# Optimization experiments

Hardware: AMD Instinct MI355X
Metric: run time of the kernel (lower is better)

## Reference

```python
import jax, jax.numpy as jnp
import numpy as np

N = 256        # SSM state size
D_MODEL = 2048 # number of independent channels sharing the kernel
L_MAX = 4096   # sequence length


def setup_inputs() -> dict:
    key = jax.random.key(0)
    k1, k2, k3, k4 = jax.random.split(key, 4)
    s = float(np.sqrt(N))
    # Stable A: eigenvalues with negative real part so A^l stays bounded after
    # bilinear discretization with step = 1/L.
    A = 0.5 * jax.random.normal(k1, (N, N), jnp.float32) / s - jnp.eye(N, dtype=jnp.float32)
    B = jax.random.normal(k2, (N, 1), jnp.float32) / s   # lecun-scale
    C = jax.random.normal(k3, (1, N), jnp.float32) / s
    D = jnp.ones((1,), jnp.float32)
    y = jax.random.normal(k4, (D_MODEL, L_MAX), jnp.float32)
    return {"y": y, "A": A, "B": B, "C": C, "D": D}


def _build_kernel(A, B, C, L, step):
    # Bilinear (Tustin) discretization, as in discretize_SSM.
    I = jnp.eye(A.shape[0], dtype=A.dtype)
    BL = jnp.linalg.inv(I - (step / 2.0) * A)
    Abar = BL @ (I + (step / 2.0) * A)
    Bbar = (BL * step) @ B                      # (N, 1)
    # K[l] = C @ Abar^l @ Bbar, computed as L matvecs via scan
    # (same math as the matrix_power loop, without O(L*N^3) cost).
    def step_fn(x, _):
        return Abar @ x, (C @ x)[0]
    _, K = jax.lax.scan(step_fn, Bbar[:, 0], None, length=L)
    return K                                     # (L,)


def _causal_conv(y, K):
    # mode='full' convolution truncated to first L samples == causal conv.
    L = y.shape[-1]
    n = 2 * L
    Yf = jnp.fft.rfft(y, n=n, axis=-1)           # (d_model, n//2+1)
    Kf = jnp.fft.rfft(K, n=n)                    # (n//2+1,)
    return jnp.fft.irfft(Yf * Kf, n=n, axis=-1)[..., :L]


def reference(y, A, B, C, D):
    L = y.shape[-1]
    K = _build_kernel(A, B, C, L, step=1.0 / L)
    return _causal_conv(y, K) + D * y
```

## Files before the change

### kernel.cpp

```cpp
#include <hip/hip_runtime.h>

#define N_ 256
#define L_ 4096
#define DM_ 2048
#define STEPF (1.0f / 4096.0f)
#define NW 15
#define NV 6
#define RQN 4608

typedef short bf16x8 __attribute__((ext_vector_type(8)));
typedef float f32x4 __attribute__((ext_vector_type(4)));
typedef unsigned int uint32;

__device__ __forceinline__ uint32 bf16rne(float f) {
    uint32 u = __builtin_bit_cast(uint32, f);
    return (u + 0x7FFFu + ((u >> 16) & 1u)) >> 16;
}
__device__ __forceinline__ float rdlane(float v, int l) {
    return __builtin_bit_cast(float, __builtin_amdgcn_readlane(__builtin_bit_cast(int, v), l));
}
__device__ __forceinline__ float hif(float x) {
    return __builtin_bit_cast(float, __builtin_bit_cast(uint32, x) & 0xFFFF0000u);
}
#define PK2(LO, HI) __builtin_amdgcn_perm(__builtin_bit_cast(uint32, (HI)), \
                                          __builtin_bit_cast(uint32, (LO)), 0x07060302u)

__global__ __launch_bounds__(1024) void k_build(const float* __restrict__ Araw,
                                                const float* __restrict__ Bv,
                                                const float* __restrict__ Cv,
                                                uint2* __restrict__ Rqg) {
    __shared__ float sm[39168];
    float* kry = sm;
    float* red = sm + 3840;
    float* Wl  = sm + 5888;
    float* Vt  = sm + 22528;
    float* Kf  = sm;

    const int tid = threadIdx.x;
    const int j = tid & 255, seg = tid >> 8, lane = tid & 63;
    const int e = 64 * seg + lane;
    float a[64];

#define DOT64(S0, S1, VV) { \
    _Pragma("unroll") \
    for (int m = 0; m < 64; m += 2) { \
        S0 = fmaf(rdlane(VV, m), a[m], S0); \
        S1 = fmaf(rdlane(VV, m + 1), a[m + 1], S1); \
    } }

#pragma unroll
    for (int m = 0; m < 64; ++m) a[m] = Araw[(64 * seg + m) * 256 + j];
    if (tid < 256) kry[tid] = Cv[tid];
    __syncthreads();
    const float WSC = 4032.0f / 4096.0f;
    {
        float vv = kry[e];
        for (int n = 1; n < NW; ++n) {
            float s0 = 0.f, s1 = 0.f;
            DOT64(s0, s1, vv)
            float* rb = red + (n & 1) * 1024;
            rb[seg * 256 + j] = s0 + s1;
            __syncthreads();
            float sc = WSC / (float)n;
            vv = (rb[e] + rb[256 + e] + rb[512 + e] + rb[768 + e]) * sc;
            if (tid < 256)
                kry[n * 256 + tid] = (rb[tid] + rb[256 + tid] + rb[512 + tid] + rb[768 + tid]) * sc;
        }
    }
    __syncthreads();
    {
        float kj[NW];
#pragma unroll
        for (int n = 0; n < NW; ++n) kj[n] = kry[n * 256 + j];
#pragma unroll
        for (int u = 0; u < 16; ++u) {
            int q = seg + 4 * u;
            float c = (float)q * (1.0f / 63.0f);
            float h = kj[NW - 1];
#pragma unroll
            for (int n = NW - 2; n >= 0; --n) h = fmaf(c, h, kj[n]);
            Wl[q * 260 + j] = h;
        }
    }

    {
        const float4* Ar = (const float4*)(Araw + (size_t)j * 256 + 64 * seg);
#pragma unroll
        for (int m4 = 0; m4 < 16; ++m4) {
            float4 q4 = Ar[m4];
            a[4 * m4] = q4.x; a[4 * m4 + 1] = q4.y; a[4 * m4 + 2] = q4.z; a[4 * m4 + 3] = q4.w;
        }
    }
    const float ms = 0.5f * STEPF;
    const float bve = Bv[e];
    {
        float vv = bve;
        for (int it = 0; it < 3; ++it) {
            float s0 = 0.f, s1 = 0.f;
            DOT64(s0, s1, vv)
            float* rb = red + (it & 1) * 1024;
            rb[seg * 256 + j] = s0 + s1;
            __syncthreads();
            vv = fmaf(ms, rb[e] + rb[256 + e] + rb[512 + e] + rb[768 + e], bve);
            if (it == 2 && tid < 256) {
                float su = rb[tid] + rb[256 + tid] + rb[512 + tid] + rb[768 + tid];
                kry[tid] = STEPF * fmaf(ms, su, Bv[tid]);
            }
        }
    }
    __syncthreads();
    const float VSC = 63.0f / 4096.0f;
    {
        float vv = kry[e];
        for (int n = 1; n < NV; ++n) {
            float s0 = 0.f, s1 = 0.f;
            DOT64(s0, s1, vv)
            float* rb = red + (n & 1) * 1024;
            rb[seg * 256 + j] = s0 + s1;
            __syncthreads();
            float sc = VSC / (float)n;
            vv = (rb[e] + rb[256 + e] + rb[512 + e] + rb[768 + e]) * sc;
            if (tid < 256)
                kry[n * 256 + tid] = (rb[tid] + rb[256 + tid] + rb[512 + tid] + rb[768 + tid]) * sc;
        }
    }
    __syncthreads();
    {
        float kj[NV];
#pragma unroll
        for (int n = 0; n < NV; ++n) kj[n] = kry[n * 256 + j];
#pragma unroll
        for (int u = 0; u < 16; ++u) {
            int r = seg + 4 * u;
            float c = (float)r * (1.0f / 63.0f);
            float h = kj[NV - 1];
#pragma unroll
            for (int n = NV - 2; n >= 0; --n) h = fmaf(c, h, kj[n]);
            Vt[r * 260 + j] = h;
        }
    }
    __syncthreads();

    {
        const int wv = tid >> 6;
        const int qt = wv >> 2, rt = wv & 3;
        const int n16 = lane & 15, g4 = lane >> 4;
        const int q = 16 * qt + n16;
        const int r = 16 * rt + n16;
        f32x4 ac = (f32x4){0.f, 0.f, 0.f, 0.f};
        for (int s = 0; s < 8; ++s) {
            const int kk = 32 * s + 8 * g4;
            float4 w0 = *(const float4*)&Wl[q * 260 + kk];
            float4 w1 = *(const float4*)&Wl[q * 260 + kk + 4];
            float4 v0 = *(const float4*)&Vt[r * 260 + kk];
            float4 v1 = *(const float4*)&Vt[r * 260 + kk + 4];
            uint4 uh; uh.x = PK2(w0.x, w0.y); uh.y = PK2(w0.z, w0.w);
                      uh.z = PK2(w1.x, w1.y); uh.w = PK2(w1.z, w1.w);
            float l0 = w0.x - hif(w0.x), l1 = w0.y - hif(w0.y);
            float l2 = w0.z - hif(w0.z), l3 = w0.w - hif(w0.w);
            float l4 = w1.x - hif(w1.x), l5 = w1.y - hif(w1.y);
            float l6 = w1.z - hif(w1.z), l7 = w1.w - hif(w1.w);
            uint4 ul; ul.x = PK2(l0, l1); ul.y = PK2(l2, l3);
                      ul.z = PK2(l4, l5); ul.w = PK2(l6, l7);
            uint4 uv; uv.x = PK2(v0.x, v0.y); uv.y = PK2(v0.z, v0.w);
                      uv.z = PK2(v1.x, v1.y); uv.w = PK2(v1.z, v1.w);
            ac = __builtin_amdgcn_mfma_f32_16x16x32_bf16(__builtin_bit_cast(bf16x8, uh),
                                                         __builtin_bit_cast(bf16x8, uv), ac, 0, 0, 0);
            ac = __builtin_amdgcn_mfma_f32_16x16x32_bf16(__builtin_bit_cast(bf16x8, ul),
                                                         __builtin_bit_cast(bf16x8, uv), ac, 0, 0, 0);
        }
#pragma unroll
        for (int jj = 0; jj < 4; ++jj)
            Kf[(16 * qt + 4 * g4 + jj) * 64 + r] = ac[jj];
    }
    __syncthreads();

    for (int i = tid; i < RQN; i += 1024) {
        int aa = 4095 - i;
        uint32 e0 = (aa >= 0) ? bf16rne(Kf[aa]) : 0u;
        uint32 e1 = (aa >= 1) ? bf16rne(Kf[aa - 1]) : 0u;
        uint32 e2 = (aa >= 2) ? bf16rne(Kf[aa - 2]) : 0u;
        uint32 e3 = (aa >= 3) ? bf16rne(Kf[aa - 3]) : 0u;
        uint2 v; v.x = e0 | (e1 << 16); v.y = e2 | (e3 << 16);
        Rqg[i] = v;
    }
#undef DOT64
}

__global__ __launch_bounds__(256, 2) void k_conv(const uint2* __restrict__ Rqg,
                                                 const float* __restrict__ y,
                                                 const float* __restrict__ Dp,
                                                 float* __restrict__ out) {
    __shared__ uint2 Rq[RQN];
    __shared__ f32x4 mbuf[2][8][64];
    const int tid = threadIdx.x;
#pragma unroll
    for (int i = 0; i < RQN / 256; ++i) Rq[i * 256 + tid] = Rqg[i * 256 + tid];
    __syncthreads();

    const int w = tid >> 6, lane = tid & 63;
    const int n = lane & 15, g = lane >> 4;
    const int ds = w & 1, jh = w >> 1;
    const int by = (int)blockIdx.y;
    const int d0w = (int)blockIdx.x * 32 + ds * 16;
    const int d = d0w + n;
    const float4* __restrict__ yq = (const float4*)(y + (size_t)d * L_);
    const float D0 = Dp[0];

#define LOADF(SL, I0) { \
    uint2 u0 = Rq[(I0)]; uint2 u1 = Rq[(I0) + 4]; \
    uint4 uu; uu.x = u0.x; uu.y = u0.y; uu.z = u1.x; uu.w = u1.y; \
    fr[SL] = __builtin_bit_cast(bf16x8, uu); }
#define PACKAV(Q0, Q1) { \
    uint4 ua; ua.x = PK2((Q0).x, (Q0).y); ua.y = PK2((Q0).z, (Q0).w); \
    ua.z = PK2((Q1).x, (Q1).y); ua.w = PK2((Q1).z, (Q1).w); \
    av = __builtin_bit_cast(bf16x8, ua); }
#define MF(TI, SL) acc[TI] = __builtin_amdgcn_mfma_f32_16x16x32_bf16(av, fr[SL], acc[TI], 0, 0, 0);

#define STEPB(YI, S0,S1,S2,S3,S4,S5,S6,S7,S8,S9,S10,S11,S12,S13,S14,S15) { \
    PACKAV(q0a, q0b); \
    q0a = q1a; q0b = q1b; \
    MF(14, S14) MF(15, S15) \
    LOADF(S14, bcur + 32) LOADF(S15, bcur + 16) \
    q1a = yq[(YI)]; q1b = yq[(YI) + 1]; \
    yn += 8; bcur += 32; \
    MF(0,S0) MF(1,S1) MF(2,S2) MF(3,S3) MF(4,S4) MF(5,S5) MF(6,S6) MF(7,S7) \
    MF(8,S8) MF(9,S9) MF(10,S10) MF(11,S11) MF(12,S12) MF(13,S13) \
}

#define ROUND8(YIM) \
    STEPB(YIM, 0,1,2,3,4,5,6,7,8,9,10,11,12,13,14,15) \
    STEPB(YIM, 14,15,0,1,2,3,4,5,6,7,8,9,10,11,12,13) \
    STEPB(YIM, 12,13,14,15,0,1,2,3,4,5,6,7,8,9,10,11) \
    STEPB(YIM, 10,11,12,13,14,15,0,1,2,3,4,5,6,7,8,9) \
    STEPB(YIM, 8,9,10,11,12,13,14,15,0,1,2,3,4,5,6,7) \
    STEPB(YIM, 6,7,8,9,10,11,12,13,14,15,0,1,2,3,4,5) \
    STEPB(YIM, 4,5,6,7,8,9,10,11,12,13,14,15,0,1,2,3) \
    STEPB(YIM, 2,3,4,5,6,7,8,9,10,11,12,13,14,15,0,1)

#define ROUND4(YIM) \
    STEPB(YIM, 0,1,2,3,4,5,6,7,8,9,10,11,12,13,14,15) \
    STEPB(YIM, 14,15,0,1,2,3,4,5,6,7,8,9,10,11,12,13) \
    STEPB(YIM, 12,13,14,15,0,1,2,3,4,5,6,7,8,9,10,11) \
    STEPB(YIM, 10,11,12,13,14,15,0,1,2,3,4,5,6,7,8,9)

    for (int strip = 0; strip < 2; ++strip) {
        const int v = strip ? by : (15 - by);
        const int t0 = v << 8;
        const int Sh = 4 * (v + 1);
        const int s0 = jh * Sh;

        f32x4 acc[16];
#pragma unroll
        for (int i = 0; i < 16; ++i) acc[i] = (f32x4){0.f, 0.f, 0.f, 0.f};
        bf16x8 fr[16], av;
        float4 q0a, q0b, q1a, q1b;

        const int B0 = 4095 - t0 - n + 8 * g + 32 * s0;
#pragma unroll
        for (int ti = 0; ti < 16; ++ti) LOADF(ti, B0 - 16 * ti)
        q0a = yq[8 * s0 + 2 * g];     q0b = yq[8 * s0 + 2 * g + 1];
        q1a = yq[8 * s0 + 8 + 2 * g]; q1b = yq[8 * s0 + 8 + 2 * g + 1];
        int bcur = B0;
        int yn = 8 * s0 + 16 + 2 * g;

        const int n8 = Sh >> 3;
        for (int it = 0; it < n8 - 1; ++it) {
            ROUND8(yn)
        }
        if (n8 > 0) {
            ROUND8(yn < 1016 ? yn : 1016)
        }
        if (Sh & 4) {
            ROUND4(yn)
        }

#pragma unroll
        for (int rr = 0; rr < 2; ++rr) {
            if (jh == 1) {
#pragma unroll
                for (int i = 0; i < 8; ++i) mbuf[ds][i][lane] = acc[rr * 8 + i];
            }
            __syncthreads();
            if (jh == 0) {
#pragma unroll
                for (int i = 0; i < 8; ++i) {
                    f32x4 m = mbuf[ds][i][lane];
                    acc[rr * 8 + i][0] += m[0]; acc[rr * 8 + i][1] += m[1];
                    acc[rr * 8 + i][2] += m[2]; acc[rr * 8 + i][3] += m[3];
                }
            }
            __syncthreads();
        }
        if (jh == 0) {
#pragma unroll
            for (int ti = 0; ti < 16; ++ti) {
                int tcol = t0 + 16 * ti + n;
#pragma unroll
                for (int r = 0; r < 4; ++r) {
                    int dr = d0w + 4 * g + r;
                    size_t ix = (size_t)dr * L_ + tcol;
                    out[ix] = acc[ti][r] + D0 * y[ix];
                }
            }
        }
    }

#undef ROUND8
#undef ROUND4
#undef STEPB
#undef MF
#undef PACKAV
#undef LOADF
}


extern "C" void kernel_launch(void* const* d_in, const int* in_sizes, int n_in,
                              void* d_out, int out_size, void* d_ws, size_t ws_size,
                              hipStream_t stream) {
    const float* y  = (const float*)d_in[0];
    const float* A  = (const float*)d_in[1];
    const float* Bv = (const float*)d_in[2];
    const float* Cv = (const float*)d_in[3];
    const float* Dp = (const float*)d_in[4];
    float* out = (float*)d_out;
    uint2* Rqg = (uint2*)d_ws;

    k_build<<<dim3(1), dim3(1024), 0, stream>>>(A, Bv, Cv, Rqg);
    k_conv<<<dim3(64, 8), dim3(256), 0, stream>>>(Rqg, y, Dp, out);

    (void)in_sizes; (void)n_in; (void)out_size; (void)ws_size;
}
```

Measured before the change: 79.92 us.

## Halve time tile to 128, widen blocks to 64 channels with 8 waves

The conv kernel now uses 512-thread blocks covering 64 channels (4 channel groups × 2 K-halves) and 128-sample output time tiles instead of 256. The grid becomes 32×16 with 16 triangular strip pairs. Each wave holds 8 accumulators and 8 Toeplitz fragments instead of 16, which lowers register pressure and allows more occupancy, and the staged Rq table in LDS is shared by more waves. In exchange each y load feeds fewer MFMAs, so reuse per load drops and there are more loop iterations and reductions.

New measurement: 107.3 us. +34.2%, slower.

```diff
diff --git a/kernel.cpp b/kernel.cpp
--- a/kernel.cpp
+++ b/kernel.cpp
@@ -187,22 +187,22 @@
 #undef DOT64
 }
 
-__global__ __launch_bounds__(256, 2) void k_conv(const uint2* __restrict__ Rqg,
+__global__ __launch_bounds__(512, 4) void k_conv(const uint2* __restrict__ Rqg,
                                                  const float* __restrict__ y,
                                                  const float* __restrict__ Dp,
                                                  float* __restrict__ out) {
     __shared__ uint2 Rq[RQN];
-    __shared__ f32x4 mbuf[2][8][64];
+    __shared__ f32x4 mbuf[4][8][64];
     const int tid = threadIdx.x;
 #pragma unroll
-    for (int i = 0; i < RQN / 256; ++i) Rq[i * 256 + tid] = Rqg[i * 256 + tid];
+    for (int i = 0; i < RQN / 512; ++i) Rq[i * 512 + tid] = Rqg[i * 512 + tid];
     __syncthreads();
 
     const int w = tid >> 6, lane = tid & 63;
     const int n = lane & 15, g = lane >> 4;
-    const int ds = w & 1, jh = w >> 1;
+    const int ds = w & 3, jh = w >> 2;
     const int by = (int)blockIdx.y;
-    const int d0w = (int)blockIdx.x * 32 + ds * 16;
+    const int d0w = (int)blockIdx.x * 64 + ds * 16;
     const int d = d0w + n;
     const float4* __restrict__ yq = (const float4*)(y + (size_t)d * L_);
     const float D0 = Dp[0];
@@ -217,84 +217,78 @@
     av = __builtin_bit_cast(bf16x8, ua); }
 #define MF(TI, SL) acc[TI] = __builtin_amdgcn_mfma_f32_16x16x32_bf16(av, fr[SL], acc[TI], 0, 0, 0);
 
-#define STEPB(YI, S0,S1,S2,S3,S4,S5,S6,S7,S8,S9,S10,S11,S12,S13,S14,S15) { \
+#define STEPE(YI, S0,S1,S2,S3,S4,S5,S6,S7) { \
     PACKAV(q0a, q0b); \
-    q0a = q1a; q0b = q1b; \
-    MF(14, S14) MF(15, S15) \
-    LOADF(S14, bcur + 32) LOADF(S15, bcur + 16) \
+    MF(6, S6) MF(7, S7) \
+    LOADF(S6, bcur + 32) LOADF(S7, bcur + 16) \
+    q0a = yq[(YI)]; q0b = yq[(YI) + 1]; \
+    yn += 8; bcur += 32; \
+    MF(0,S0) MF(1,S1) MF(2,S2) MF(3,S3) MF(4,S4) MF(5,S5) \
+}
+#define STEPO(YI, S0,S1,S2,S3,S4,S5,S6,S7) { \
+    PACKAV(q1a, q1b); \
+    MF(6, S6) MF(7, S7) \
+    LOADF(S6, bcur + 32) LOADF(S7, bcur + 16) \
     q1a = yq[(YI)]; q1b = yq[(YI) + 1]; \
     yn += 8; bcur += 32; \
-    MF(0,S0) MF(1,S1) MF(2,S2) MF(3,S3) MF(4,S4) MF(5,S5) MF(6,S6) MF(7,S7) \
-    MF(8,S8) MF(9,S9) MF(10,S10) MF(11,S11) MF(12,S12) MF(13,S13) \
-}
-
-#define ROUND8(YIM) \
-    STEPB(YIM, 0,1,2,3,4,5,6,7,8,9,10,11,12,13,14,15) \
-    STEPB(YIM, 14,15,0,1,2,3,4,5,6,7,8,9,10,11,12,13) \
-    STEPB(YIM, 12,13,14,15,0,1,2,3,4,5,6,7,8,9,10,11) \
-    STEPB(YIM, 10,11,12,13,14,15,0,1,2,3,4,5,6,7,8,9) \
-    STEPB(YIM, 8,9,10,11,12,13,14,15,0,1,2,3,4,5,6,7) \
-    STEPB(YIM, 6,7,8,9,10,11,12,13,14,15,0,1,2,3,4,5) \
-    STEPB(YIM, 4,5,6,7,8,9,10,11,12,13,14,15,0,1,2,3) \
-    STEPB(YIM, 2,3,4,5,6,7,8,9,10,11,12,13,14,15,0,1)
+    MF(0,S0) MF(1,S1) MF(2,S2) MF(3,S3) MF(4,S4) MF(5,S5) \
+}
 
 #define ROUND4(YIM) \
-    STEPB(YIM, 0,1,2,3,4,5,6,7,8,9,10,11,12,13,14,15) \
-    STEPB(YIM, 14,15,0,1,2,3,4,5,6,7,8,9,10,11,12,13) \
-    STEPB(YIM, 12,13,14,15,0,1,2,3,4,5,6,7,8,9,10,11) \
-    STEPB(YIM, 10,11,12,13,14,15,0,1,2,3,4,5,6,7,8,9)
+    STEPE(YIM, 0,1,2,3,4,5,6,7) \
+    STEPO(YIM, 6,7,0,1,2,3,4,5) \
+    STEPE(YIM, 4,5,6,7,0,1,2,3) \
+    STEPO(YIM, 2,3,4,5,6,7,0,1)
 
     for (int strip = 0; strip < 2; ++strip) {
-        const int v = strip ? by : (15 - by);
-        const int t0 = v << 8;
-        const int Sh = 4 * (v + 1);
+        const int v = strip ? by : (31 - by);
+        const int t0 = v << 7;
+        const int Sh = 2 * (v + 1);
         const int s0 = jh * Sh;
 
-        f32x4 acc[16];
-#pragma unroll
-        for (int i = 0; i < 16; ++i) acc[i] = (f32x4){0.f, 0.f, 0.f, 0.f};
-        bf16x8 fr[16], av;
+        f32x4 acc[8];
+#pragma unroll
+        for (int i = 0; i < 8; ++i) acc[i] = (f32x4){0.f, 0.f, 0.f, 0.f};
+        bf16x8 fr[8], av;
         float4 q0a, q0b, q1a, q1b;
 
         const int B0 = 4095 - t0 - n + 8 * g + 32 * s0;
 #pragma unroll
-        for (int ti = 0; ti < 16; ++ti) LOADF(ti, B0 - 16 * ti)
+        for (int ti = 0; ti < 8; ++ti) LOADF(ti, B0 - 16 * ti)
         q0a = yq[8 * s0 + 2 * g];     q0b = yq[8 * s0 + 2 * g + 1];
         q1a = yq[8 * s0 + 8 + 2 * g]; q1b = yq[8 * s0 + 8 + 2 * g + 1];
         int bcur = B0;
         int yn = 8 * s0 + 16 + 2 * g;
 
-        const int n8 = Sh >> 3;
-        for (int it = 0; it < n8 - 1; ++it) {
-            ROUND8(yn)
-        }
-        if (n8 > 0) {
-            ROUND8(yn < 1016 ? yn : 1016)
-        }
-        if (Sh & 4) {
+        const int nfull = Sh >> 2;
+        for (int it = 0; it < nfull - 1; ++it) {
             ROUND4(yn)
         }
-
-#pragma unroll
-        for (int rr = 0; rr < 2; ++rr) {
-            if (jh == 1) {
-#pragma unroll
-                for (int i = 0; i < 8; ++i) mbuf[ds][i][lane] = acc[rr * 8 + i];
+        if (nfull > 0) {
+            ROUND4(yn < 1016 ? yn : 1016)
+        }
+        if (Sh & 2) {
+            STEPE(yn, 0,1,2,3,4,5,6,7)
+            STEPO(yn, 6,7,0,1,2,3,4,5)
+        }
+
+        if (jh == 1) {
+#pragma unroll
+            for (int i = 0; i < 8; ++i) mbuf[ds][i][lane] = acc[i];
+        }
+        __syncthreads();
+        if (jh == 0) {
+#pragma unroll
+            for (int i = 0; i < 8; ++i) {
+                f32x4 m = mbuf[ds][i][lane];
+                acc[i][0] += m[0]; acc[i][1] += m[1];
+                acc[i][2] += m[2]; acc[i][3] += m[3];
             }
-            __syncthreads();
-            if (jh == 0) {
-#pragma unroll
-                for (int i = 0; i < 8; ++i) {
-                    f32x4 m = mbuf[ds][i][lane];
-                    acc[rr * 8 + i][0] += m[0]; acc[rr * 8 + i][1] += m[1];
-                    acc[rr * 8 + i][2] += m[2]; acc[rr * 8 + i][3] += m[3];
-                }
-            }
-            __syncthreads();
-        }
+        }
+        __syncthreads();
         if (jh == 0) {
 #pragma unroll
-            for (int ti = 0; ti < 16; ++ti) {
+            for (int ti = 0; ti < 8; ++ti) {
                 int tcol = t0 + 16 * ti + n;
 #pragma unroll
                 for (int r = 0; r < 4; ++r) {
@@ -306,9 +300,9 @@
         }
     }
 
-#undef ROUND8
 #undef ROUND4
-#undef STEPB
+#undef STEPE
+#undef STEPO
 #undef MF
 #undef PACKAV
 #undef LOADF
@@ -327,7 +321,7 @@
     uint2* Rqg = (uint2*)d_ws;
 
     k_build<<<dim3(1), dim3(1024), 0, stream>>>(A, Bv, Cv, Rqg);
-    k_conv<<<dim3(64, 8), dim3(256), 0, stream>>>(Rqg, y, Dp, out);
+    k_conv<<<dim3(32, 16), dim3(512), 0, stream>>>(Rqg, y, Dp, out);
 
     (void)in_sizes; (void)n_in; (void)out_size; (void)ws_size;
 }
```

## Pre-convert y to bf16 in extra build blocks and trim kernel series terms

Applied to the files above, without the earlier changes.

Adds 256 extra blocks to the build kernel that convert y from fp32 to packed bf16 in workspace. These run alongside the single-block kernel construction. The conv kernel then loads 16-byte bf16 vectors instead of two float4s and no longer packs in its inner loop, which halves y read traffic in the hot loop and removes the tail clamp logic. The series truncation orders (NW, NV, and the resolvent iterations) are also reduced to shorten the serial build phase. The risks are lower accuracy in the kernel taps and an extra global write and read of y.

Measured after the change: 68.31 us. 14.5% less time.

```diff
diff --git a/kernel.cpp b/kernel.cpp
--- a/kernel.cpp
+++ b/kernel.cpp
@@ -4,8 +4,8 @@
 #define L_ 4096
 #define DM_ 2048
 #define STEPF (1.0f / 4096.0f)
-#define NW 15
-#define NV 6
+#define NW 10
+#define NV 5
 #define RQN 4608
 
 typedef short bf16x8 __attribute__((ext_vector_type(8)));
@@ -28,7 +28,25 @@
 __global__ __launch_bounds__(1024) void k_build(const float* __restrict__ Araw,
                                                 const float* __restrict__ Bv,
                                                 const float* __restrict__ Cv,
-                                                uint2* __restrict__ Rqg) {
+                                                const float* __restrict__ yf,
+                                                uint2* __restrict__ Rqg,
+                                                uint4* __restrict__ ybf) {
+    const int tid = threadIdx.x;
+    if (blockIdx.x > 0) {
+        const size_t base = (size_t)(blockIdx.x - 1) * 32768;
+        const float4* yin = (const float4*)(yf + base);
+        uint4* yo = ybf + base / 8;
+#pragma unroll
+        for (int i = 0; i < 4; ++i) {
+            int c = i * 1024 + tid;
+            float4 q0 = yin[2 * c], q1 = yin[2 * c + 1];
+            uint4 o; o.x = PK2(q0.x, q0.y); o.y = PK2(q0.z, q0.w);
+                     o.z = PK2(q1.x, q1.y); o.w = PK2(q1.z, q1.w);
+            yo[c] = o;
+        }
+        return;
+    }
+
     __shared__ float sm[39168];
     float* kry = sm;
     float* red = sm + 3840;
@@ -36,7 +54,6 @@
     float* Vt  = sm + 22528;
     float* Kf  = sm;
 
-    const int tid = threadIdx.x;
     const int j = tid & 255, seg = tid >> 8, lane = tid & 63;
     const int e = 64 * seg + lane;
     float a[64];
@@ -95,14 +112,14 @@
     const float bve = Bv[e];
     {
         float vv = bve;
-        for (int it = 0; it < 3; ++it) {
+        for (int it = 0; it < 2; ++it) {
             float s0 = 0.f, s1 = 0.f;
             DOT64(s0, s1, vv)
             float* rb = red + (it & 1) * 1024;
             rb[seg * 256 + j] = s0 + s1;
             __syncthreads();
             vv = fmaf(ms, rb[e] + rb[256 + e] + rb[512 + e] + rb[768 + e], bve);
-            if (it == 2 && tid < 256) {
+            if (it == 1 && tid < 256) {
                 float su = rb[tid] + rb[256 + tid] + rb[512 + tid] + rb[768 + tid];
                 kry[tid] = STEPF * fmaf(ms, su, Bv[tid]);
             }
@@ -188,6 +205,7 @@
 }
 
 __global__ __launch_bounds__(256, 2) void k_conv(const uint2* __restrict__ Rqg,
+                                                 const uint4* __restrict__ ybf,
                                                  const float* __restrict__ y,
                                                  const float* __restrict__ Dp,
                                                  float* __restrict__ out) {
@@ -204,45 +222,49 @@
     const int by = (int)blockIdx.y;
     const int d0w = (int)blockIdx.x * 32 + ds * 16;
     const int d = d0w + n;
-    const float4* __restrict__ yq = (const float4*)(y + (size_t)d * L_);
+    const uint4* __restrict__ ybr = ybf + (size_t)d * (L_ / 8);
     const float D0 = Dp[0];
 
 #define LOADF(SL, I0) { \
     uint2 u0 = Rq[(I0)]; uint2 u1 = Rq[(I0) + 4]; \
     uint4 uu; uu.x = u0.x; uu.y = u0.y; uu.z = u1.x; uu.w = u1.y; \
     fr[SL] = __builtin_bit_cast(bf16x8, uu); }
-#define PACKAV(Q0, Q1) { \
-    uint4 ua; ua.x = PK2((Q0).x, (Q0).y); ua.y = PK2((Q0).z, (Q0).w); \
-    ua.z = PK2((Q1).x, (Q1).y); ua.w = PK2((Q1).z, (Q1).w); \
-    av = __builtin_bit_cast(bf16x8, ua); }
 #define MF(TI, SL) acc[TI] = __builtin_amdgcn_mfma_f32_16x16x32_bf16(av, fr[SL], acc[TI], 0, 0, 0);
 
-#define STEPB(YI, S0,S1,S2,S3,S4,S5,S6,S7,S8,S9,S10,S11,S12,S13,S14,S15) { \
-    PACKAV(q0a, q0b); \
-    q0a = q1a; q0b = q1b; \
+#define STEPE(S0,S1,S2,S3,S4,S5,S6,S7,S8,S9,S10,S11,S12,S13,S14,S15) { \
+    av = __builtin_bit_cast(bf16x8, ave); \
     MF(14, S14) MF(15, S15) \
     LOADF(S14, bcur + 32) LOADF(S15, bcur + 16) \
-    q1a = yq[(YI)]; q1b = yq[(YI) + 1]; \
-    yn += 8; bcur += 32; \
+    ave = ybr[yn & 511]; \
+    yn += 4; bcur += 32; \
     MF(0,S0) MF(1,S1) MF(2,S2) MF(3,S3) MF(4,S4) MF(5,S5) MF(6,S6) MF(7,S7) \
     MF(8,S8) MF(9,S9) MF(10,S10) MF(11,S11) MF(12,S12) MF(13,S13) \
 }
-
-#define ROUND8(YIM) \
-    STEPB(YIM, 0,1,2,3,4,5,6,7,8,9,10,11,12,13,14,15) \
-    STEPB(YIM, 14,15,0,1,2,3,4,5,6,7,8,9,10,11,12,13) \
-    STEPB(YIM, 12,13,14,15,0,1,2,3,4,5,6,7,8,9,10,11) \
-    STEPB(YIM, 10,11,12,13,14,15,0,1,2,3,4,5,6,7,8,9) \
-    STEPB(YIM, 8,9,10,11,12,13,14,15,0,1,2,3,4,5,6,7) \
-    STEPB(YIM, 6,7,8,9,10,11,12,13,14,15,0,1,2,3,4,5) \
-    STEPB(YIM, 4,5,6,7,8,9,10,11,12,13,14,15,0,1,2,3) \
-    STEPB(YIM, 2,3,4,5,6,7,8,9,10,11,12,13,14,15,0,1)
-
-#define ROUND4(YIM) \
-    STEPB(YIM, 0,1,2,3,4,5,6,7,8,9,10,11,12,13,14,15) \
-    STEPB(YIM, 14,15,0,1,2,3,4,5,6,7,8,9,10,11,12,13) \
-    STEPB(YIM, 12,13,14,15,0,1,2,3,4,5,6,7,8,9,10,11) \
-    STEPB(YIM, 10,11,12,13,14,15,0,1,2,3,4,5,6,7,8,9)
+#define STEPO(S0,S1,S2,S3,S4,S5,S6,S7,S8,S9,S10,S11,S12,S13,S14,S15) { \
+    av = __builtin_bit_cast(bf16x8, avo); \
+    MF(14, S14) MF(15, S15) \
+    LOADF(S14, bcur + 32) LOADF(S15, bcur + 16) \
+    avo = ybr[yn & 511]; \
+    yn += 4; bcur += 32; \
+    MF(0,S0) MF(1,S1) MF(2,S2) MF(3,S3) MF(4,S4) MF(5,S5) MF(6,S6) MF(7,S7) \
+    MF(8,S8) MF(9,S9) MF(10,S10) MF(11,S11) MF(12,S12) MF(13,S13) \
+}
+
+#define ROUND8() \
+    STEPE(0,1,2,3,4,5,6,7,8,9,10,11,12,13,14,15) \
+    STEPO(14,15,0,1,2,3,4,5,6,7,8,9,10,11,12,13) \
+    STEPE(12,13,14,15,0,1,2,3,4,5,6,7,8,9,10,11) \
+    STEPO(10,11,12,13,14,15,0,1,2,3,4,5,6,7,8,9) \
+    STEPE(8,9,10,11,12,13,14,15,0,1,2,3,4,5,6,7) \
+    STEPO(6,7,8,9,10,11,12,13,14,15,0,1,2,3,4,5) \
+    STEPE(4,5,6,7,8,9,10,11,12,13,14,15,0,1,2,3) \
+    STEPO(2,3,4,5,6,7,8,9,10,11,12,13,14,15,0,1)
+
+#define ROUND4() \
+    STEPE(0,1,2,3,4,5,6,7,8,9,10,11,12,13,14,15) \
+    STEPO(14,15,0,1,2,3,4,5,6,7,8,9,10,11,12,13) \
+    STEPE(12,13,14,15,0,1,2,3,4,5,6,7,8,9,10,11) \
+    STEPO(10,11,12,13,14,15,0,1,2,3,4,5,6,7,8,9)
 
     for (int strip = 0; strip < 2; ++strip) {
         const int v = strip ? by : (15 - by);
@@ -254,25 +276,22 @@
 #pragma unroll
         for (int i = 0; i < 16; ++i) acc[i] = (f32x4){0.f, 0.f, 0.f, 0.f};
         bf16x8 fr[16], av;
-        float4 q0a, q0b, q1a, q1b;
+        uint4 ave, avo;
 
         const int B0 = 4095 - t0 - n + 8 * g + 32 * s0;
 #pragma unroll
         for (int ti = 0; ti < 16; ++ti) LOADF(ti, B0 - 16 * ti)
-        q0a = yq[8 * s0 + 2 * g];     q0b = yq[8 * s0 + 2 * g + 1];
-        q1a = yq[8 * s0 + 8 + 2 * g]; q1b = yq[8 * s0 + 8 + 2 * g + 1];
+        ave = ybr[4 * s0 + g];
+        avo = ybr[4 * s0 + 4 + g];
         int bcur = B0;
-        int yn = 8 * s0 + 16 + 2 * g;
+        int yn = 4 * s0 + 8 + g;
 
         const int n8 = Sh >> 3;
-        for (int it = 0; it < n8 - 1; ++it) {
-            ROUND8(yn)
-        }
-        if (n8 > 0) {
-            ROUND8(yn < 1016 ? yn : 1016)
+        for (int it = 0; it < n8; ++it) {
+            ROUND8()
         }
         if (Sh & 4) {
-            ROUND4(yn)
+            ROUND4()
         }
 
 #pragma unroll
@@ -308,9 +327,9 @@
 
 #undef ROUND8
 #undef ROUND4
-#undef STEPB
+#undef STEPE
+#undef STEPO
 #undef MF
-#undef PACKAV
 #undef LOADF
 }
 
@@ -324,10 +343,12 @@
     const float* Cv = (const float*)d_in[3];
     const float* Dp = (const float*)d_in[4];
     float* out = (float*)d_out;
-    uint2* Rqg = (uint2*)d_ws;
-
-    k_build<<<dim3(1), dim3(1024), 0, stream>>>(A, Bv, Cv, Rqg);
-    k_conv<<<dim3(64, 8), dim3(256), 0, stream>>>(Rqg, y, Dp, out);
+    char* w = (char*)d_ws;
+    uint2* Rqg = (uint2*)w;
+    uint4* ybf = (uint4*)(w + 36864);
+
+    k_build<<<dim3(257), dim3(1024), 0, stream>>>(A, Bv, Cv, y, Rqg, ybf);
+    k_conv<<<dim3(64, 8), dim3(256), 0, stream>>>(Rqg, ybf, y, Dp, out);
 
     (void)in_sizes; (void)n_in; (void)out_size; (void)ws_size;
 }
```
